# Kernel optimization log

Measured on AMD Instinct MI355X. Metric: run time of the kernel, lower is better.

The kernel has to match this reference:

```python
import jax, jax.numpy as jnp
import numpy as np

B, T, D, H, L, F = 128, 512, 32, 128, 3, 4


def setup_inputs() -> dict:
    key = jax.random.key(0)
    ks = jax.random.split(key, 13)
    s = 0.05
    inp = {
        "x": jax.random.normal(ks[0], (B, T, D), dtype=jnp.float32),
        # layer 0 input weights [4H, D]; layers 1..L-1 input weights [L-1, 4H, H]
        "w_ih0": jax.random.normal(ks[1], (4 * H, D), dtype=jnp.float32) * s,
        "w_ih_rest": jax.random.normal(ks[2], (L - 1, 4 * H, H), dtype=jnp.float32) * s,
        "w_hh": jax.random.normal(ks[3], (L, 4 * H, H), dtype=jnp.float32) * s,
        "b_ih": jax.random.normal(ks[4], (L, 4 * H), dtype=jnp.float32) * s,
        "b_hh": jax.random.normal(ks[5], (L, 4 * H), dtype=jnp.float32) * s,
        "w_attn": jax.random.normal(ks[6], (1, H), dtype=jnp.float32) * s,
        "b_attn": jax.random.normal(ks[7], (1,), dtype=jnp.float32) * s,
        "w1": jax.random.normal(ks[8], (64, H), dtype=jnp.float32) * s,
        "b1": jax.random.normal(ks[9], (64,), dtype=jnp.float32) * s,
        "w2": jax.random.normal(ks[10], (F, 64), dtype=jnp.float32) * s,
        "b2": jax.random.normal(ks[11], (F,), dtype=jnp.float32) * s,
    }
    return inp


def _lstm_layer(xs, w_ih, w_hh, bi, bh):
    # xs: [B, T, Din] -> hs: [B, T, H]; PyTorch gate order i, f, g, o
    b, t = xs.shape[0], xs.shape[1]
    h_dim = w_hh.shape[1]
    pre = jnp.einsum('bti,gi->btg', xs, w_ih) + bi + bh  # [B, T, 4H]

    def step(carry, p_t):
        h, c = carry
        g = p_t + h @ w_hh.T
        i, f, gg, o = jnp.split(g, 4, axis=-1)
        i = jax.nn.sigmoid(i)
        f = jax.nn.sigmoid(f)
        gg = jnp.tanh(gg)
        o = jax.nn.sigmoid(o)
        c = f * c + i * gg
        h = o * jnp.tanh(c)
        return (h, c), h

    h0 = jnp.zeros((b, h_dim), xs.dtype)
    _, hs = jax.lax.scan(step, (h0, h0), jnp.swapaxes(pre, 0, 1))
    return jnp.swapaxes(hs, 0, 1)


def reference(x, w_ih0, w_ih_rest, w_hh, b_ih, b_hh, w_attn, b_attn, w1, b1, w2, b2):
    out = _lstm_layer(x, w_ih0, w_hh[0], b_ih[0], b_hh[0])
    for l in range(1, L):
        out = _lstm_layer(out, w_ih_rest[l - 1], w_hh[l], b_ih[l], b_hh[l])
    # additive attention pooling over time
    attn_w = jax.nn.softmax(jnp.einsum('bth,oh->bto', out, w_attn) + b_attn, axis=1)  # [B,T,1]
    ctx = jnp.sum(attn_w * out, axis=1)  # [B, H]
    # MLP head (dropout is identity at inference)
    h1 = jax.nn.relu(ctx @ w1.T + b1)
    return h1 @ w2.T + b2
```

## Files before the change

kernel.cpp:

```cpp
#include <hip/hip_runtime.h>
#include <math.h>

#define Bn 128
#define Tn 512
#define Dn 32
#define Hn 128
#define Gn 512
#define Ln 3

#define BAR_LDS() asm volatile("s_waitcnt lgkmcnt(0)\n\ts_barrier" ::: "memory")

typedef _Float16 h2 __attribute__((ext_vector_type(2)));
typedef _Float16 half8 __attribute__((ext_vector_type(8)));
typedef float f32x4 __attribute__((ext_vector_type(4)));

__device__ __forceinline__ float dot2(h2 a, h2 b, float c) {
    return __builtin_amdgcn_fdot2(a, b, c, false);
}
__device__ __forceinline__ h2 pkh(float a, float b) {
    h2 r; r.x = (_Float16)a; r.y = (_Float16)b; return r;
}
__device__ __forceinline__ float sigm(float x) {
    return __builtin_amdgcn_rcpf(1.f + __expf(-x));
}
__device__ __forceinline__ float tanh_fast(float x) {
    return 1.f - 2.f * __builtin_amdgcn_rcpf(1.f + __expf(2.f * x));
}

#define DPPADD(a, CTRL) { \
    int _t = __builtin_amdgcn_update_dpp(0, __builtin_bit_cast(int, a), \
                                         CTRL, 0xF, 0xF, true); \
    a += __builtin_bit_cast(float, _t); }

#define KEEPH(x) asm volatile("" : "+v"(x))
#define LD8H(p) (*(const half8*)(p))
#define H2OF(V, i) (((const h2*)&(V))[i])

#define DECL16(P, R) \
  h2 P##0=pkh((R)[0],(R)[1]),   P##1=pkh((R)[2],(R)[3]),   P##2=pkh((R)[4],(R)[5]),   P##3=pkh((R)[6],(R)[7]),   \
     P##4=pkh((R)[8],(R)[9]),   P##5=pkh((R)[10],(R)[11]), P##6=pkh((R)[12],(R)[13]), P##7=pkh((R)[14],(R)[15]), \
     P##8=pkh((R)[16],(R)[17]), P##9=pkh((R)[18],(R)[19]), P##10=pkh((R)[20],(R)[21]),P##11=pkh((R)[22],(R)[23]),\
     P##12=pkh((R)[24],(R)[25]),P##13=pkh((R)[26],(R)[27]),P##14=pkh((R)[28],(R)[29]),P##15=pkh((R)[30],(R)[31]);
#define KEEP16(P) \
  KEEPH(P##0); KEEPH(P##1); KEEPH(P##2); KEEPH(P##3); KEEPH(P##4); KEEPH(P##5); \
  KEEPH(P##6); KEEPH(P##7); KEEPH(P##8); KEEPH(P##9); KEEPH(P##10); KEEPH(P##11); \
  KEEPH(P##12); KEEPH(P##13); KEEPH(P##14); KEEPH(P##15);

#define EXTRACT16(P, A, B, C, D) \
  h2 P##0 = H2OF(A,0), P##1 = H2OF(A,1), P##2  = H2OF(A,2), P##3  = H2OF(A,3), \
     P##4 = H2OF(B,0), P##5 = H2OF(B,1), P##6  = H2OF(B,2), P##7  = H2OF(B,3), \
     P##8 = H2OF(C,0), P##9 = H2OF(C,1), P##10 = H2OF(C,2), P##11 = H2OF(C,3), \
     P##12= H2OF(D,0), P##13= H2OF(D,1), P##14 = H2OF(D,2), P##15 = H2OF(D,3);

#define DOTA(j) { \
    aI = dot2(hvA##j, wiA##j, aI);  aF = dot2(hvA##j, wfA##j, aF); \
    aG = dot2(hvA##j, wgA##j, aG);  aO = dot2(hvA##j, woA##j, aO); }
#define DOTB(j) { \
    aI = dot2(hvB##j, wiB##j, aI);  aF = dot2(hvB##j, wfB##j, aF); \
    aG = dot2(hvB##j, wgB##j, aG);  aO = dot2(hvB##j, woB##j, aO); }

__global__ __launch_bounds__(256) void cvt_f2h(
    const float* __restrict__ in, _Float16* __restrict__ out, int n)
{
    int base = (blockIdx.x * 256 + threadIdx.x) * 4;
    if (base < n) {
        float4 v = *(const float4*)(in + base);
        *(h2*)(out + base)     = pkh(v.x, v.y);
        *(h2*)(out + base + 2) = pkh(v.z, v.w);
    }
}

__global__ __launch_bounds__(256) void gemm_pre_mfma(
    const _Float16* __restrict__ A, int K, int rowStrideB, int t0, int tlog,
    const _Float16* __restrict__ W,
    const float* __restrict__ bi, const float* __restrict__ bh,
    _Float16* __restrict__ C)
{
    __shared__ h2 As2[64][20];
    __shared__ h2 Bs2[64][20];
    const int tid  = threadIdx.x;
    const int row0 = blockIdx.x * 64;
    const int col0 = blockIdx.y * 64;
    const int w    = tid >> 6;
    const int lane = tid & 63;
    const int qm   = (w >> 1) * 32;
    const int qn   = (w & 1) * 32;
    const int fm   = lane & 15;
    const int fq   = lane >> 4;
    const int tmask = (1 << tlog) - 1;
    const int lrow = tid >> 2;
    const int lk   = (tid & 3) * 8;

    f32x4 acc00 = {0,0,0,0}, acc01 = {0,0,0,0};
    f32x4 acc10 = {0,0,0,0}, acc11 = {0,0,0,0};

    for (int k0 = 0; k0 < K; k0 += 32) {
        {
            int rg = row0 + lrow;
            int b_idx = rg >> tlog, tt = rg & tmask;
            const _Float16* ap = A + (size_t)b_idx * rowStrideB +
                                 (size_t)(t0 + tt) * K + (k0 + lk);
            *(float4*)&As2[lrow][(tid & 3) * 4] = *(const float4*)ap;
            const _Float16* wp = W + (size_t)(col0 + lrow) * K + (k0 + lk);
            *(float4*)&Bs2[lrow][(tid & 3) * 4] = *(const float4*)wp;
        }
        __syncthreads();
        half8 a0 = *(const half8*)&As2[qm + fm][fq * 4];
        half8 a1 = *(const half8*)&As2[qm + 16 + fm][fq * 4];
        half8 b0 = *(const half8*)&Bs2[qn + fm][fq * 4];
        half8 b1 = *(const half8*)&Bs2[qn + 16 + fm][fq * 4];
        acc00 = __builtin_amdgcn_mfma_f32_16x16x32_f16(a0, b0, acc00, 0, 0, 0);
        acc01 = __builtin_amdgcn_mfma_f32_16x16x32_f16(a0, b1, acc01, 0, 0, 0);
        acc10 = __builtin_amdgcn_mfma_f32_16x16x32_f16(a1, b0, acc10, 0, 0, 0);
        acc11 = __builtin_amdgcn_mfma_f32_16x16x32_f16(a1, b1, acc11, 0, 0, 0);
        __syncthreads();
    }

    const int g0 = col0 + qn + fm;
    const int g1 = g0 + 16;
    const float bb0 = bi[g0] + bh[g0];
    const float bb1 = bi[g1] + bh[g1];
    const int m0 = row0 + qm + fq * 4;
    #pragma unroll
    for (int r = 0; r < 4; r++) {
        C[(size_t)(m0 + r) * Gn + g0]      = (_Float16)(acc00[r] + bb0);
        C[(size_t)(m0 + r) * Gn + g1]      = (_Float16)(acc01[r] + bb1);
        C[(size_t)(m0 + 16 + r) * Gn + g0] = (_Float16)(acc10[r] + bb0);
        C[(size_t)(m0 + 16 + r) * Gn + g1] = (_Float16)(acc11[r] + bb1);
    }
}

__global__ __launch_bounds__(256)
__attribute__((amdgpu_waves_per_eu(1, 2)))
void scan256(
    const _Float16* __restrict__ pre,
    const float* __restrict__ w_hh,
    _Float16* __restrict__ hs16)
{
    const int b    = blockIdx.x;
    const int tid  = threadIdx.x;
    const int lane = tid & 63;
    const int wv   = tid >> 6;
    const int kq   = lane & 1;
    const int u    = wv * 32 + (lane >> 1);

    __shared__ h2 hbuf[2][Hn / 2];
    __shared__ float lds_pad[20480];

    if (pre == nullptr) {
        lds_pad[tid] = (float)tid;
        __syncthreads();
        ((float*)hs16)[tid] = lds_pad[(tid * 7) & 20479];
    }

    const float* rI = w_hh + (size_t)(0 * Hn + u) * Hn + kq * 64;
    const float* rF = w_hh + (size_t)(1 * Hn + u) * Hn + kq * 64;
    const float* rG = w_hh + (size_t)(2 * Hn + u) * Hn + kq * 64;
    const float* rO = w_hh + (size_t)(3 * Hn + u) * Hn + kq * 64;
    DECL16(wiA, rI) DECL16(wiB, (rI + 32))
    DECL16(wfA, rF) DECL16(wfB, (rF + 32))
    DECL16(wgA, rG) DECL16(wgB, (rG + 32))
    DECL16(woA, rO) DECL16(woB, (rO + 32))
    KEEP16(wiA) KEEP16(wiB) KEEP16(wfA) KEEP16(wfB)
    KEEP16(wgA) KEEP16(wgB) KEEP16(woA) KEEP16(woB)

    if (tid < Hn / 2) hbuf[0][tid] = pkh(0.f, 0.f);
    __syncthreads();

    const _Float16* pp = pre + (size_t)b * Tn * Gn + u;
    _Float16* hswr = hs16 + (size_t)b * Tn * Hn + u;

    const float ms = (kq == 0) ? 1.f : 0.f;

    float pI0 = ms * (float)pp[0],      pF0 = ms * (float)pp[Hn];
    float pG0 = ms * (float)pp[2 * Hn], pO0 = ms * (float)pp[3 * Hn];
    float pI1 = ms * (float)pp[Gn],     pF1 = ms * (float)pp[Gn + Hn];
    float pG1 = ms * (float)pp[Gn + 2 * Hn], pO1 = ms * (float)pp[Gn + 3 * Hn];
    const _Float16* pld = pp + 2 * (size_t)Gn;

    float cr = 0.f;

    auto body = [&](int t, float vI, float vF, float vG, float vO) {
        const h2* hrow = &hbuf[t & 1][kq * 32];
        half8 hA = LD8H(hrow);      half8 hB = LD8H(hrow + 4);
        half8 hC = LD8H(hrow + 8);  half8 hD = LD8H(hrow + 12);
        half8 hE = LD8H(hrow + 16); half8 hF_ = LD8H(hrow + 20);
        half8 hG_ = LD8H(hrow + 24); half8 hH_ = LD8H(hrow + 28);
        EXTRACT16(hvA, hA, hB, hC, hD)
        EXTRACT16(hvB, hE, hF_, hG_, hH_)

        float aI = vI, aF = vF, aG = vG, aO = vO;
        DOTA(0)  DOTA(1)  DOTA(2)  DOTA(3)
        DOTA(4)  DOTA(5)  DOTA(6)  DOTA(7)
        DOTA(8)  DOTA(9)  DOTA(10) DOTA(11)
        DOTA(12) DOTA(13) DOTA(14) DOTA(15)
        DOTB(0)  DOTB(1)  DOTB(2)  DOTB(3)
        DOTB(4)  DOTB(5)  DOTB(6)  DOTB(7)
        DOTB(8)  DOTB(9)  DOTB(10) DOTB(11)
        DOTB(12) DOTB(13) DOTB(14) DOTB(15)

        DPPADD(aI, 0xB1) DPPADD(aF, 0xB1) DPPADD(aG, 0xB1) DPPADD(aO, 0xB1)

        float iv = sigm(aI);
        float fv = sigm(aF);
        float gv = tanh_fast(aG);
        float ov = sigm(aO);
        cr = fv * cr + iv * gv;
        float hnew = ov * tanh_fast(cr);
        _Float16 hh = (_Float16)hnew;
        if (kq == 0) {
            ((_Float16*)hbuf[(t + 1) & 1])[u] = hh;
            *hswr = hh;
        }
        hswr += Hn;
        BAR_LDS();
    };

    const int TN2 = Tn - 2;
    for (int t = 0; t < TN2; t++) {
        float vI = pI0, vF = pF0, vG = pG0, vO = pO0;
        pI0 = pI1; pF0 = pF1; pG0 = pG1; pO0 = pO1;
        pI1 = ms * (float)pld[0];      pF1 = ms * (float)pld[Hn];
        pG1 = ms * (float)pld[2 * Hn]; pO1 = ms * (float)pld[3 * Hn];
        pld += Gn;
        body(t, vI, vF, vG, vO);
    }
    {
        float vI = pI0, vF = pF0, vG = pG0, vO = pO0;
        pI0 = pI1; pF0 = pF1; pG0 = pG1; pO0 = pO1;
        body(TN2, vI, vF, vG, vO);
    }
    body(TN2 + 1, pI0, pF0, pG0, pO0);
}

__global__ __launch_bounds__(256) void head_kernel(
    const _Float16* __restrict__ hs16,
    const float* __restrict__ w_attn, const float* __restrict__ b_attn,
    const float* __restrict__ w1, const float* __restrict__ b1,
    const float* __restrict__ w2, const float* __restrict__ b2,
    float* __restrict__ out)
{
    const int b = blockIdx.x;
    const int tid = threadIdx.x;
    __shared__ h2 wa2[Hn / 2];
    __shared__ __align__(16) float sc[Tn];
    __shared__ __align__(16) float red[256];
    __shared__ __align__(16) float ctx_sh[Hn];
    __shared__ __align__(16) float h1_sh[64];

    if (tid < Hn / 2) wa2[tid] = pkh(w_attn[2 * tid], w_attn[2 * tid + 1]);
    __syncthreads();

    const _Float16* hb = hs16 + (size_t)b * Tn * Hn;

    for (int t = tid; t < Tn; t += 256) {
        const h2* hp = (const h2*)(hb + (size_t)t * Hn);
        float s = 0.f;
        #pragma unroll
        for (int k = 0; k < 64; k++) s = dot2(hp[k], wa2[k], s);
        sc[t] = s + b_attn[0];
    }
    __syncthreads();

    float m = fmaxf(sc[tid], sc[tid + 256]);
    red[tid] = m; __syncthreads();
    for (int s_ = 128; s_ > 0; s_ >>= 1) {
        if (tid < s_) red[tid] = fmaxf(red[tid], red[tid + s_]);
        __syncthreads();
    }
    float mx = red[0];
    __syncthreads();
    float e0 = __expf(sc[tid] - mx), e1 = __expf(sc[tid + 256] - mx);
    sc[tid] = e0; sc[tid + 256] = e1;
    red[tid] = e0 + e1; __syncthreads();
    for (int s_ = 128; s_ > 0; s_ >>= 1) {
        if (tid < s_) red[tid] += red[tid + s_];
        __syncthreads();
    }
    float inv = 1.f / red[0];
    __syncthreads();

    {
        int jj = tid & 127, half = tid >> 7;
        float a = 0.f;
        for (int t = half * 256; t < half * 256 + 256; t++)
            a += sc[t] * (float)hb[(size_t)t * Hn + jj];
        red[tid] = a;
        __syncthreads();
        if (tid < Hn) ctx_sh[tid] = (red[tid] + red[tid + Hn]) * inv;
        __syncthreads();
    }

    if (tid < 64) {
        const float4* wvv = (const float4*)(w1 + (size_t)tid * Hn);
        const float4* cv = (const float4*)ctx_sh;
        float s = 0.f;
        #pragma unroll
        for (int k = 0; k < 32; k++) {
            float4 a = wvv[k], c = cv[k];
            s += a.x * c.x + a.y * c.y + a.z * c.z + a.w * c.w;
        }
        h1_sh[tid] = fmaxf(s + b1[tid], 0.f);
    }
    __syncthreads();

    if (tid < 4) {
        float s = 0.f;
        const float* wvv = w2 + tid * 64;
        #pragma unroll
        for (int k = 0; k < 64; k++) s += wvv[k] * h1_sh[k];
        out[b * 4 + tid] = s + b2[tid];
    }
}

extern "C" void kernel_launch(void* const* d_in, const int* in_sizes, int n_in,
                              void* d_out, int out_size, void* d_ws, size_t ws_size,
                              hipStream_t stream)
{
    const float* x        = (const float*)d_in[0];
    const float* w_ih0    = (const float*)d_in[1];
    const float* w_ih_rest= (const float*)d_in[2];
    const float* w_hh     = (const float*)d_in[3];
    const float* b_ih     = (const float*)d_in[4];
    const float* b_hh     = (const float*)d_in[5];
    const float* w_attn   = (const float*)d_in[6];
    const float* b_attn   = (const float*)d_in[7];
    const float* w1       = (const float*)d_in[8];
    const float* b1       = (const float*)d_in[9];
    const float* w2       = (const float*)d_in[10];
    const float* b2       = (const float*)d_in[11];
    float* out = (float*)d_out;

    const size_t nX   = (size_t)Bn * Tn * Dn;
    const size_t nHS  = (size_t)Bn * Tn * Hn;
    const size_t nW0  = (size_t)Gn * Dn;
    const size_t nWR  = (size_t)(Ln - 1) * Gn * Hn;
    const size_t nPRE = (size_t)Bn * Tn * Gn;

    _Float16* preh = (_Float16*)d_ws;
    _Float16* xh   = preh + nPRE;
    _Float16* hs0  = xh + nX;
    _Float16* hs1  = hs0 + nHS;
    _Float16* hs2  = hs1 + nHS;
    _Float16* w0h  = hs2 + nHS;
    _Float16* wrh  = w0h + nW0;

    cvt_f2h<<<(int)((nX / 4 + 255) / 256), 256, 0, stream>>>(x, xh, (int)nX);
    cvt_f2h<<<(int)((nW0 / 4 + 255) / 256), 256, 0, stream>>>(w_ih0, w0h, (int)nW0);
    cvt_f2h<<<(int)((nWR / 4 + 255) / 256), 256, 0, stream>>>(w_ih_rest, wrh, (int)nWR);

    for (int l = 0; l < Ln; l++) {
        const _Float16* A = (l == 0) ? xh : (l == 1 ? hs0 : hs1);
        int K = (l == 0) ? Dn : Hn;
        const _Float16* W = (l == 0) ? w0h : (wrh + (size_t)(l - 1) * Gn * Hn);
        _Float16* hsOut = (l == 0) ? hs0 : (l == 1 ? hs1 : hs2);

        gemm_pre_mfma<<<dim3(Bn * Tn / 64, 8), 256, 0, stream>>>(
            A, K, Tn * K, 0, 9, W, b_ih + l * Gn, b_hh + l * Gn, preh);
        scan256<<<Bn, 256, 0, stream>>>(
            preh, w_hh + (size_t)l * Gn * Hn, hsOut);
    }

    head_kernel<<<Bn, 256, 0, stream>>>(hs2, w_attn, b_attn, w1, b1, w2, b2, out);
}
```

Measured before the change: 1.082 ms.

## Fuse fp32-to-fp16 conversion into GEMM and interleave pre-activations by timestep pairs

Removes the three separate conversion kernels by converting fp32 x and input weights to fp16 inside the GEMM tile load. The GEMM output is stored with two consecutive timesteps interleaved, so the recurrent scan fetches one packed half2 per gate for every two steps, halving its global load count. The scan loop is restructured to process timestep pairs. In exchange, the GEMM reads fp32 weights repeatedly and its output stores become strided 2-byte writes.

```diff
diff --git a/kernel.cpp b/kernel.cpp
--- a/kernel.cpp
+++ b/kernel.cpp
@@ -59,20 +59,10 @@
     aI = dot2(hvB##j, wiB##j, aI);  aF = dot2(hvB##j, wfB##j, aF); \
     aG = dot2(hvB##j, wgB##j, aG);  aO = dot2(hvB##j, woB##j, aO); }
 
-__global__ __launch_bounds__(256) void cvt_f2h(
-    const float* __restrict__ in, _Float16* __restrict__ out, int n)
-{
-    int base = (blockIdx.x * 256 + threadIdx.x) * 4;
-    if (base < n) {
-        float4 v = *(const float4*)(in + base);
-        *(h2*)(out + base)     = pkh(v.x, v.y);
-        *(h2*)(out + base + 2) = pkh(v.z, v.w);
-    }
-}
-
-__global__ __launch_bounds__(256) void gemm_pre_mfma(
-    const _Float16* __restrict__ A, int K, int rowStrideB, int t0, int tlog,
-    const _Float16* __restrict__ W,
+template<typename TA>
+__global__ __launch_bounds__(256) void gemm_pre(
+    const TA* __restrict__ A, int K, int rowStrideB, int t0, int tlog,
+    const float* __restrict__ W,
     const float* __restrict__ bi, const float* __restrict__ bh,
     _Float16* __restrict__ C)
 {
@@ -98,11 +88,29 @@
         {
             int rg = row0 + lrow;
             int b_idx = rg >> tlog, tt = rg & tmask;
-            const _Float16* ap = A + (size_t)b_idx * rowStrideB +
-                                 (size_t)(t0 + tt) * K + (k0 + lk);
-            *(float4*)&As2[lrow][(tid & 3) * 4] = *(const float4*)ap;
-            const _Float16* wp = W + (size_t)(col0 + lrow) * K + (k0 + lk);
-            *(float4*)&Bs2[lrow][(tid & 3) * 4] = *(const float4*)wp;
+            const TA* ap = A + (size_t)b_idx * rowStrideB +
+                           (size_t)(t0 + tt) * K + (k0 + lk);
+            if constexpr (sizeof(TA) == 2) {
+                *(float4*)&As2[lrow][(tid & 3) * 4] = *(const float4*)ap;
+            } else {
+                float4 va = *(const float4*)ap;
+                float4 vb = *(const float4*)(ap + 4);
+                float4 o;
+                ((h2*)&o)[0] = pkh(va.x, va.y);
+                ((h2*)&o)[1] = pkh(va.z, va.w);
+                ((h2*)&o)[2] = pkh(vb.x, vb.y);
+                ((h2*)&o)[3] = pkh(vb.z, vb.w);
+                *(float4*)&As2[lrow][(tid & 3) * 4] = o;
+            }
+            const float* wp = W + (size_t)(col0 + lrow) * K + (k0 + lk);
+            float4 wa = *(const float4*)wp;
+            float4 wb = *(const float4*)(wp + 4);
+            float4 ow;
+            ((h2*)&ow)[0] = pkh(wa.x, wa.y);
+            ((h2*)&ow)[1] = pkh(wa.z, wa.w);
+            ((h2*)&ow)[2] = pkh(wb.x, wb.y);
+            ((h2*)&ow)[3] = pkh(wb.z, wb.w);
+            *(float4*)&Bs2[lrow][(tid & 3) * 4] = ow;
         }
         __syncthreads();
         half8 a0 = *(const half8*)&As2[qm + fm][fq * 4];
@@ -123,10 +131,11 @@
     const int m0 = row0 + qm + fq * 4;
     #pragma unroll
     for (int r = 0; r < 4; r++) {
-        C[(size_t)(m0 + r) * Gn + g0]      = (_Float16)(acc00[r] + bb0);
-        C[(size_t)(m0 + r) * Gn + g1]      = (_Float16)(acc01[r] + bb1);
-        C[(size_t)(m0 + 16 + r) * Gn + g0] = (_Float16)(acc10[r] + bb0);
-        C[(size_t)(m0 + 16 + r) * Gn + g1] = (_Float16)(acc11[r] + bb1);
+        int ma = m0 + r, mb = m0 + 16 + r;
+        C[((size_t)(ma >> 1) * Gn + g0) * 2 + (ma & 1)] = (_Float16)(acc00[r] + bb0);
+        C[((size_t)(ma >> 1) * Gn + g1) * 2 + (ma & 1)] = (_Float16)(acc01[r] + bb1);
+        C[((size_t)(mb >> 1) * Gn + g0) * 2 + (mb & 1)] = (_Float16)(acc10[r] + bb0);
+        C[((size_t)(mb >> 1) * Gn + g1) * 2 + (mb & 1)] = (_Float16)(acc11[r] + bb1);
     }
 }
 
@@ -167,16 +176,14 @@
     if (tid < Hn / 2) hbuf[0][tid] = pkh(0.f, 0.f);
     __syncthreads();
 
-    const _Float16* pp = pre + (size_t)b * Tn * Gn + u;
+    const h2* qq = (const h2*)pre + (size_t)(b * 256) * Gn + u;
     _Float16* hswr = hs16 + (size_t)b * Tn * Hn + u;
 
     const float ms = (kq == 0) ? 1.f : 0.f;
 
-    float pI0 = ms * (float)pp[0],      pF0 = ms * (float)pp[Hn];
-    float pG0 = ms * (float)pp[2 * Hn], pO0 = ms * (float)pp[3 * Hn];
-    float pI1 = ms * (float)pp[Gn],     pF1 = ms * (float)pp[Gn + Hn];
-    float pG1 = ms * (float)pp[Gn + 2 * Hn], pO1 = ms * (float)pp[Gn + 3 * Hn];
-    const _Float16* pld = pp + 2 * (size_t)Gn;
+    h2 qI0 = qq[0],        qF0 = qq[128],      qG0 = qq[256],      qO0 = qq[384];
+    h2 qI1 = qq[Gn],       qF1 = qq[Gn + 128], qG1 = qq[Gn + 256], qO1 = qq[Gn + 384];
+    const h2* pld = qq + 2 * (size_t)Gn;
 
     float cr = 0.f;
 
@@ -216,21 +223,24 @@
         BAR_LDS();
     };
 
-    const int TN2 = Tn - 2;
-    for (int t = 0; t < TN2; t++) {
-        float vI = pI0, vF = pF0, vG = pG0, vO = pO0;
-        pI0 = pI1; pF0 = pF1; pG0 = pG1; pO0 = pO1;
-        pI1 = ms * (float)pld[0];      pF1 = ms * (float)pld[Hn];
-        pG1 = ms * (float)pld[2 * Hn]; pO1 = ms * (float)pld[3 * Hn];
+    for (int pr = 0; pr < 254; pr++) {
+        body(2 * pr,     ms * (float)qI0.x, ms * (float)qF0.x,
+                         ms * (float)qG0.x, ms * (float)qO0.x);
+        body(2 * pr + 1, ms * (float)qI0.y, ms * (float)qF0.y,
+                         ms * (float)qG0.y, ms * (float)qO0.y);
+        qI0 = qI1; qF0 = qF1; qG0 = qG1; qO0 = qO1;
+        qI1 = pld[0]; qF1 = pld[128]; qG1 = pld[256]; qO1 = pld[384];
         pld += Gn;
-        body(t, vI, vF, vG, vO);
-    }
-    {
-        float vI = pI0, vF = pF0, vG = pG0, vO = pO0;
-        pI0 = pI1; pF0 = pF1; pG0 = pG1; pO0 = pO1;
-        body(TN2, vI, vF, vG, vO);
-    }
-    body(TN2 + 1, pI0, pF0, pG0, pO0);
+    }
+    body(508, ms * (float)qI0.x, ms * (float)qF0.x,
+              ms * (float)qG0.x, ms * (float)qO0.x);
+    body(509, ms * (float)qI0.y, ms * (float)qF0.y,
+              ms * (float)qG0.y, ms * (float)qO0.y);
+    qI0 = qI1; qF0 = qF1; qG0 = qG1; qO0 = qO1;
+    body(510, ms * (float)qI0.x, ms * (float)qF0.x,
+              ms * (float)qG0.x, ms * (float)qO0.x);
+    body(511, ms * (float)qI0.y, ms * (float)qF0.y,
+              ms * (float)qG0.y, ms * (float)qO0.y);
 }
 
 __global__ __launch_bounds__(256) void head_kernel(
@@ -331,35 +341,27 @@
     const float* b2       = (const float*)d_in[11];
     float* out = (float*)d_out;
 
-    const size_t nX   = (size_t)Bn * Tn * Dn;
     const size_t nHS  = (size_t)Bn * Tn * Hn;
-    const size_t nW0  = (size_t)Gn * Dn;
-    const size_t nWR  = (size_t)(Ln - 1) * Gn * Hn;
     const size_t nPRE = (size_t)Bn * Tn * Gn;
 
     _Float16* preh = (_Float16*)d_ws;
-    _Float16* xh   = preh + nPRE;
-    _Float16* hs0  = xh + nX;
+    _Float16* hs0  = preh + nPRE;
     _Float16* hs1  = hs0 + nHS;
     _Float16* hs2  = hs1 + nHS;
-    _Float16* w0h  = hs2 + nHS;
-    _Float16* wrh  = w0h + nW0;
-
-    cvt_f2h<<<(int)((nX / 4 + 255) / 256), 256, 0, stream>>>(x, xh, (int)nX);
-    cvt_f2h<<<(int)((nW0 / 4 + 255) / 256), 256, 0, stream>>>(w_ih0, w0h, (int)nW0);
-    cvt_f2h<<<(int)((nWR / 4 + 255) / 256), 256, 0, stream>>>(w_ih_rest, wrh, (int)nWR);
-
-    for (int l = 0; l < Ln; l++) {
-        const _Float16* A = (l == 0) ? xh : (l == 1 ? hs0 : hs1);
-        int K = (l == 0) ? Dn : Hn;
-        const _Float16* W = (l == 0) ? w0h : (wrh + (size_t)(l - 1) * Gn * Hn);
-        _Float16* hsOut = (l == 0) ? hs0 : (l == 1 ? hs1 : hs2);
-
-        gemm_pre_mfma<<<dim3(Bn * Tn / 64, 8), 256, 0, stream>>>(
-            A, K, Tn * K, 0, 9, W, b_ih + l * Gn, b_hh + l * Gn, preh);
-        scan256<<<Bn, 256, 0, stream>>>(
-            preh, w_hh + (size_t)l * Gn * Hn, hsOut);
-    }
+
+    gemm_pre<float><<<dim3(Bn * Tn / 64, 8), 256, 0, stream>>>(
+        x, Dn, Tn * Dn, 0, 9, w_ih0, b_ih, b_hh, preh);
+    scan256<<<Bn, 256, 0, stream>>>(preh, w_hh, hs0);
+
+    gemm_pre<_Float16><<<dim3(Bn * Tn / 64, 8), 256, 0, stream>>>(
+        hs0, Hn, Tn * Hn, 0, 9, w_ih_rest,
+        b_ih + Gn, b_hh + Gn, preh);
+    scan256<<<Bn, 256, 0, stream>>>(preh, w_hh + (size_t)Gn * Hn, hs1);
+
+    gemm_pre<_Float16><<<dim3(Bn * Tn / 64, 8), 256, 0, stream>>>(
+        hs1, Hn, Tn * Hn, 0, 9, w_ih_rest + (size_t)Gn * Hn,
+        b_ih + 2 * Gn, b_hh + 2 * Gn, preh);
+    scan256<<<Bn, 256, 0, stream>>>(preh, w_hh + 2 * (size_t)Gn * Hn, hs2);
 
     head_kernel<<<Bn, 256, 0, stream>>>(hs2, w_attn, b_attn, w1, b1, w2, b2, out);
 }
```

Measured after the change: 1.011 ms. 6.6% less time.
